# Optimization experiments

Hardware: AMD Instinct MI355X
Metric: run time of the kernel (lower is better)

## Reference

```python
import jax, jax.numpy as jnp
import numpy as np

T, B, S = 128, 64, 256
H, E, V = 1024, 512, 32000
PAD_ID = 0

def setup_inputs() -> dict:
    key = jax.random.key(0)
    ks = jax.random.split(key, 12)
    sc = lambda *sh: 1.0 / np.sqrt(sh[-1])
    return {
        'target_ids': jax.random.randint(ks[0], (T, B), 0, V, dtype=jnp.int32),
        'visual_context': jax.random.normal(ks[1], (B, S, 2 * H), jnp.float32),
        'h0': jax.random.normal(ks[2], (B, H), jnp.float32),
        'c0': jax.random.normal(ks[3], (B, H), jnp.float32),
        'E_tgt': jax.random.normal(ks[4], (V, E), jnp.float32) * 0.02,
        'W_att': jax.random.normal(ks[5], (H, 2 * H), jnp.float32) * sc(2 * H),
        'b_att': jnp.zeros((H,), jnp.float32),
        'W_ih': jax.random.normal(ks[6], (4 * H, E + H), jnp.float32) * sc(E + H),
        'W_hh': jax.random.normal(ks[7], (4 * H, H), jnp.float32) * sc(H),
        'W_u': jax.random.normal(ks[8], (H, 3 * H), jnp.float32) * sc(3 * H),
        'W_vocab': jax.random.normal(ks[9], (V, H), jnp.float32) * sc(H),
        'b_vocab': jnp.zeros((V,), jnp.float32),
    }

def reference(target_ids, visual_context, h0, c0, E_tgt, W_att, b_att,
              W_ih, W_hh, W_u, W_vocab, b_vocab):
    # enc_hidden_proj = att_projection(visual_context): (B, S, H)
    enc_proj = jnp.einsum('bsd,hd->bsh', visual_context, W_att) + b_att
    Y = E_tgt[target_ids[:-1]]  # (T-1, B, E) — teacher-forced inputs

    def step(carry, Y_t):
        h, c, o_prev = carry
        Ybar = jnp.concatenate([o_prev, Y_t], axis=1)  # (B, H+E)
        gates = Ybar @ W_ih.T + h @ W_hh.T             # (B, 4H), no bias
        i, f, g, o = jnp.split(gates, 4, axis=1)       # torch LSTMCell order
        i = jax.nn.sigmoid(i); f = jax.nn.sigmoid(f)
        g = jnp.tanh(g); o = jax.nn.sigmoid(o)
        c = f * c + i * g
        h = o * jnp.tanh(c)
        e_t = jnp.einsum('bsh,bh->bs', enc_proj, h)    # attention scores
        alpha = jax.nn.softmax(e_t, axis=1)
        a_t = jnp.einsum('bs,bsd->bd', alpha, visual_context)  # (B, 2H)
        u_t = jnp.concatenate([a_t, h], axis=1)        # (B, 3H)
        o_t = jnp.tanh(u_t @ W_u.T)                    # dropout = identity (eval)
        return (h, c, o_t), o_t

    o_init = jnp.zeros((h0.shape[0], W_u.shape[0]), h0.dtype)
    _, combined = jax.lax.scan(step, (h0, c0, o_init), Y)  # (T-1, B, H)

    logits = jnp.einsum('tbh,vh->tbv', combined, W_vocab) + b_vocab
    P = jax.nn.log_softmax(logits, axis=-1)            # (T-1, B, V)
    gold = target_ids[1:]                              # (T-1, B)
    gold_lp = jnp.take_along_axis(P, gold[..., None].astype(jnp.int32), axis=-1)[..., 0]
    mask = (gold != PAD_ID).astype(P.dtype)
    scores = (gold_lp * mask).sum(axis=0)              # (B,)
    return scores
```

## Files before the change

kernel.cpp:

```cpp
#include <hip/hip_runtime.h>
#include <hip/hip_bf16.h>

#define TSTEPS 127
#define NBLK 256
#define NVB 250
#define MROWS 8128

typedef unsigned short u16;
typedef unsigned int u32;
typedef unsigned long long u64;
typedef _Float16 f16;
typedef __attribute__((ext_vector_type(8))) short bf16x8;
typedef __attribute__((ext_vector_type(8))) _Float16 f16x8;
typedef __attribute__((ext_vector_type(8))) unsigned short u16x8;
typedef __attribute__((ext_vector_type(4))) float f32x4;

__device__ __forceinline__ u16 f2h(float f){ f16 h=(f16)f; u16 r; __builtin_memcpy(&r,&h,2); return r; }
__device__ __forceinline__ float h2f(u16 u){ f16 h; __builtin_memcpy(&h,&u,2); return (float)h; }
__device__ __forceinline__ float us2f(u16 u){ union{float f;u32 i;}v; v.i=(u32)u<<16; return v.f; }
__device__ __forceinline__ u16 f2us(float f){ __hip_bfloat16 h=__float2bfloat16(f); u16 r; __builtin_memcpy(&r,&h,2); return r; }
__device__ __forceinline__ void split2(float x, u16& hi, u16& lo){
  u16 h = f2us(x); lo = f2us(x - us2f(h)); hi = h;
}

__device__ __forceinline__ u64 ldg64(const u64* p){
  return __hip_atomic_load((u64*)p, __ATOMIC_RELAXED, __HIP_MEMORY_SCOPE_AGENT);
}
__device__ __forceinline__ float ldgf(const float* p){
  return __hip_atomic_load((float*)p, __ATOMIC_RELAXED, __HIP_MEMORY_SCOPE_AGENT);
}
__device__ __forceinline__ void stg64(u64* p, u64 v){
  __hip_atomic_store(p, v, __ATOMIC_RELAXED, __HIP_MEMORY_SCOPE_AGENT);
}
__device__ __forceinline__ void stg32(u32* p, u32 v){
  __hip_atomic_store(p, v, __ATOMIC_RELAXED, __HIP_MEMORY_SCOPE_AGENT);
}
__device__ __forceinline__ void stgf(float* p, float v){
  __hip_atomic_store(p, v, __ATOMIC_RELAXED, __HIP_MEMORY_SCOPE_AGENT);
}
__device__ __forceinline__ f16x8 mk8h(u64 a, u64 b){
  union { u64 q[2]; f16x8 v; } u; u.q[0]=a; u.q[1]=b; return u.v;
}

__device__ __forceinline__ void gbar(u32* flags, u32 token){
  asm volatile("s_waitcnt vmcnt(0) lgkmcnt(0)" ::: "memory");
  __syncthreads();
  if (threadIdx.x == 0)
    __hip_atomic_store(&flags[blockIdx.x*32], token, __ATOMIC_RELAXED, __HIP_MEMORY_SCOPE_AGENT);
  u32* myf = &flags[threadIdx.x*32];
  while (__hip_atomic_load(myf, __ATOMIC_RELAXED, __HIP_MEMORY_SCOPE_AGENT) < token)
    __builtin_amdgcn_s_sleep(1);
  __syncthreads();
}

__global__ void p_wcat(const float* __restrict__ Watt, const float* __restrict__ Wu,
                       float* __restrict__ Wcat){
  int idx = blockIdx.x*256 + threadIdx.x;
  int n = idx >> 11, k = idx & 2047;
  Wcat[idx] = (n < 1024) ? Watt[idx] : Wu[(size_t)(n-1024)*3072 + k];
}

__global__ void p_wy(const float* __restrict__ Wih, u16* __restrict__ WYh, u16* __restrict__ WYl){
  int k = blockIdx.x*256 + threadIdx.x;
  int rp = blockIdx.y;
  int j = (rp & 3)*1024 + (rp >> 2);
  float v = Wih[(size_t)j*1536 + 1024 + k];
  u16 hi, lo; split2(v, hi, lo);
  WYh[(size_t)rp*512 + k] = hi; WYl[(size_t)rp*512 + k] = lo;
}

__global__ void p_wuh(const float* __restrict__ Wu, u16* __restrict__ Wh){
  int k = blockIdx.x*256 + threadIdx.x;
  int j = blockIdx.y;
  Wh[(size_t)j*1024 + k] = f2h(Wu[(size_t)j*3072 + 2048 + k]);
}

__global__ void p_y(const int* __restrict__ ids, const float* __restrict__ Etgt,
                    u16* __restrict__ Yh, u16* __restrict__ Yl){
  int e0 = blockIdx.x*256 + threadIdx.x;
  int row = blockIdx.y;
  int id = ids[row];
  float v = Etgt[(size_t)id*512 + e0];
  u16 hi, lo; split2(v, hi, lo);
  Yh[(size_t)row*512 + e0] = hi; Yl[(size_t)row*512 + e0] = lo;
}

__global__ void p_wv(const float* __restrict__ Wv, u16* __restrict__ Wvb){
  size_t idx = (size_t)blockIdx.x*256 + threadIdx.x;
  Wvb[idx] = f2h(Wv[idx]);
}

__global__ void p_init(const float* __restrict__ h0,
                       u16* __restrict__ hf, u16* __restrict__ of,
                       u32* __restrict__ flags){
  int idx = blockIdx.x*256 + threadIdx.x;
  if (idx < 65536){
    hf[idx] = f2h(h0[idx]);
    of[idx] = 0;
  } else if (idx < 65536 + 8192){
    flags[idx - 65536] = 0;
  }
}

union SharedU {
  struct { u16 a[128*72]; u16 b[128*72]; } st;
  float cc[128*128];
};

__global__ __launch_bounds__(256) void k_gemm32(
    const float* __restrict__ A, const float* __restrict__ Bm,
    const float* __restrict__ bias, u16* __restrict__ ep, u16* __restrict__ vu)
{
  __shared__ SharedU sm;
  const int tid = threadIdx.x;
  const int lane = tid & 63, w = tid >> 6;
  const int wm = w >> 1, wn = w & 1;
  int lw = blockIdx.y * gridDim.x + blockIdx.x;
  int swz = (lw & 7)*256 + (lw >> 3);
  const int n0 = (swz & 15) * 128, m0 = (swz >> 4) * 128;
  f32x4 acc[4][4];
#pragma unroll
  for (int i=0;i<4;i++)
#pragma unroll
    for (int j=0;j<4;j++) acc[i][j] = (f32x4)(0.f);

  for (int k0 = 0; k0 < 2048; k0 += 64) {
    __syncthreads();
#pragma unroll
    for (int i=0;i<8;i++){
      int idx = tid + i*256;
      int r = idx >> 4, c4 = idx & 15;
      float4 va = *(const float4*)(&A[(size_t)(m0+r)*2048 + k0 + c4*4]);
      ushort4 sa; sa.x=f2h(va.x); sa.y=f2h(va.y); sa.z=f2h(va.z); sa.w=f2h(va.w);
      *(ushort4*)(&sm.st.a[r*72 + c4*4]) = sa;
      float4 vb = *(const float4*)(&Bm[(size_t)(n0+r)*2048 + k0 + c4*4]);
      ushort4 sb; sb.x=f2h(vb.x); sb.y=f2h(vb.y); sb.z=f2h(vb.z); sb.w=f2h(vb.w);
      *(ushort4*)(&sm.st.b[r*72 + c4*4]) = sb;
    }
    __syncthreads();
#pragma unroll
    for (int kk = 0; kk < 64; kk += 32) {
      f16x8 af[4], bfr[4];
      int krow = kk + ((lane >> 4) << 3);
#pragma unroll
      for (int m4=0;m4<4;m4++)
        af[m4] = *(const f16x8*)(&sm.st.a[(wm*64 + m4*16 + (lane & 15))*72 + krow]);
#pragma unroll
      for (int n4=0;n4<4;n4++)
        bfr[n4] = *(const f16x8*)(&sm.st.b[(wn*64 + n4*16 + (lane & 15))*72 + krow]);
#pragma unroll
      for (int m4=0;m4<4;m4++)
#pragma unroll
        for (int n4=0;n4<4;n4++)
          acc[m4][n4] = __builtin_amdgcn_mfma_f32_16x16x32_f16(af[m4], bfr[n4], acc[m4][n4], 0,0,0);
    }
  }
  __syncthreads();
#pragma unroll
  for (int m4=0;m4<4;m4++)
#pragma unroll
    for (int n4=0;n4<4;n4++)
#pragma unroll
      for (int i=0;i<4;i++){
        int row = wm*64 + m4*16 + ((lane>>4)<<2) + i;
        int col = wn*64 + n4*16 + (lane&15);
        sm.cc[row*128 + col] = acc[m4][n4][i];
      }
  __syncthreads();
  for (int idx = tid; idx < 128*128; idx += 256) {
    int row = idx >> 7, col = idx & 127;
    int gm = m0 + row, gn = n0 + col;
    float vv = sm.cc[idx];
    if (gn < 1024) { vv += bias[gn]; ep[(size_t)gm*1024 + gn] = f2h(vv); }
    else           { vu[(size_t)gm*1024 + (gn-1024)] = f2h(vv); }
  }
}

__global__ __launch_bounds__(256) void k_gy(
    const u16* __restrict__ Ah, const u16* __restrict__ Al,
    const u16* __restrict__ Bh, const u16* __restrict__ Bl,
    float* __restrict__ gY)
{
  __shared__ u16 sah[128*40], sal[128*40], sbh[128*40], sbl[128*40];
  const int tid = threadIdx.x;
  const int lane = tid & 63, w = tid >> 6;
  const int wm = w >> 1, wn = w & 1;
  const int l15 = lane & 15, q8 = (lane>>4)*8;
  int lw = blockIdx.y * gridDim.x + blockIdx.x;
  int swz = (lw & 7)*256 + (lw >> 3);
  const int n0 = (swz & 31)*128, m0 = (swz >> 5)*128;
  f32x4 acc[4][4];
#pragma unroll
  for (int i=0;i<4;i++)
#pragma unroll
    for (int j=0;j<4;j++) acc[i][j] = (f32x4)(0.f);

  for (int k0 = 0; k0 < 512; k0 += 32){
    __syncthreads();
#pragma unroll
    for (int i=0;i<8;i++){
      int idx = i*256 + tid;
      int mat = idx >> 9, sub = idx & 511;
      int r = sub >> 2, c8 = (sub & 3)*8;
      const u16* src = (mat==0)?Ah:(mat==1)?Al:(mat==2)?Bh:Bl;
      size_t base = (mat<2 ? (size_t)(m0+r)*512 : (size_t)(n0+r)*512) + k0 + c8;
      u16x8 v = *(const u16x8*)(src + base);
      u16* dst = (mat==0)?sah:(mat==1)?sal:(mat==2)?sbh:sbl;
      *(u16x8*)(&dst[r*40 + c8]) = v;
    }
    __syncthreads();
    bf16x8 ah[4], al2[4], bh[4], bl2[4];
#pragma unroll
    for (int m4=0;m4<4;m4++){
      ah[m4]  = *(const bf16x8*)(&sah[(wm*64+m4*16+l15)*40 + q8]);
      al2[m4] = *(const bf16x8*)(&sal[(wm*64+m4*16+l15)*40 + q8]);
    }
#pragma unroll
    for (int n4=0;n4<4;n4++){
      bh[n4]  = *(const bf16x8*)(&sbh[(wn*64+n4*16+l15)*40 + q8]);
      bl2[n4] = *(const bf16x8*)(&sbl[(wn*64+n4*16+l15)*40 + q8]);
    }
#pragma unroll
    for (int m4=0;m4<4;m4++)
#pragma unroll
      for (int n4=0;n4<4;n4++){
        acc[m4][n4] = __builtin_amdgcn_mfma_f32_16x16x32_bf16(ah[m4],  bh[n4],  acc[m4][n4], 0,0,0);
        acc[m4][n4] = __builtin_amdgcn_mfma_f32_16x16x32_bf16(al2[m4], bh[n4],  acc[m4][n4], 0,0,0);
        acc[m4][n4] = __builtin_amdgcn_mfma_f32_16x16x32_bf16(ah[m4],  bl2[n4], acc[m4][n4], 0,0,0);
      }
  }
#pragma unroll
  for (int m4=0;m4<4;m4++)
#pragma unroll
    for (int n4=0;n4<4;n4++)
#pragma unroll
      for (int i=0;i<4;i++){
        int gm = m0 + wm*64 + m4*16 + ((lane>>4)<<2) + i;
        int gn = n0 + wn*64 + n4*16 + l15;
        gY[(size_t)gm*4096 + gn] = acc[m4][n4][i];
      }
}

struct LoopShared {
  u16 wg[32*2048];
  union {
    struct { float psum[2][64][8]; u32 hstage[32][4]; } p1;
    struct { float al[256]; float pared[4][256]; float red[8]; } p3;
  } u;
};

__global__ __launch_bounds__(256, 1) void k_loop(
    const float* __restrict__ Wih, const float* __restrict__ Whh,
    const float* __restrict__ c0g,
    const u16* __restrict__ Wuh16, const float* __restrict__ gY,
    const u16* __restrict__ ep, const u16* __restrict__ vuu,
    u16* __restrict__ hf, u16* __restrict__ of,
    float* __restrict__ ebuf, float* __restrict__ phB,
    u16* __restrict__ comb, u32* __restrict__ flags)
{
  __shared__ LoopShared sh;
  const int tid = threadIdx.x, blk = blockIdx.x;
  const int lane = tid & 63, w = tid >> 6;
  const int l15 = lane & 15, q = lane >> 4;
  const int jb = blk >> 1, bhalf = blk & 1;
  const int bsub = w & 1, khalf = w >> 1;
  const int b = bhalf*32 + bsub*16 + l15;

  for (int i = tid; i < 32*512; i += 256){
    int r = i >> 9, c4 = i & 511;
    int jp = jb*32 + r;
    int j  = (jp & 3)*1024 + (jp >> 2);
    float4 v = (c4 < 256) ? *(const float4*)(&Wih[(size_t)j*1536 + c4*4])
                          : *(const float4*)(&Whh[(size_t)j*1024 + (c4-256)*4]);
    ushort4 hh; hh.x=f2h(v.x); hh.y=f2h(v.y); hh.z=f2h(v.z); hh.w=f2h(v.w);
    int byteoff = (r*4096 + c4*8) ^ ((r & 7) << 4);
    *(ushort4*)((char*)sh.wg + byteoff) = hh;
  }
  float cReg0 = 0.f, cReg1 = 0.f;
  if (w < 2){
    cReg0 = c0g[(size_t)b*1024 + jb*8 + q];
    cReg1 = c0g[(size_t)b*1024 + jb*8 + 4 + q];
  }
  __syncthreads();
  const char* wgc = (const char*)sh.wg;

  for (int t = 0; t < TSTEPS; ++t){
    const int p = t & 1;
    const u16* hP = hf + p*65536;
    u16* hN = hf + (p^1)*65536;

    {
      float4 gyv0, gyv1;
      if (w < 2){
        const float* gb = gY + ((size_t)(t*64 + b))*4096 + jb*32 + q*4;
        gyv0 = *(const float4*)(gb);
        gyv1 = *(const float4*)(gb + 16);
      }
      const u64* xsrc = (khalf ? (const u64*)hP : (const u64*)of) + b*256;
      f32x4 acc0 = (f32x4)(0.f), acc1 = (f32x4)(0.f);
#pragma unroll 4
      for (int kt = 0; kt < 32; ++kt){
        int base = khalf*2048 + kt*64 + q*16;
        int w0 = (l15*4096 + base) ^ ((l15 & 7) << 4);
        f16x8 wf0 = *(const f16x8*)(wgc + w0);
        f16x8 wf1 = *(const f16x8*)(wgc + w0 + 65536);
        const u64* px = xsrc + kt*8 + q*2;
        f16x8 xf = mk8h(ldg64(px), ldg64(px+1));
        acc0 = __builtin_amdgcn_mfma_f32_16x16x32_f16(wf0, xf, acc0, 0,0,0);
        acc1 = __builtin_amdgcn_mfma_f32_16x16x32_f16(wf1, xf, acc1, 0,0,0);
      }
      if (w >= 2){
        float* ps_ = &sh.u.p1.psum[w-2][lane][0];
#pragma unroll
        for (int i=0;i<4;i++){ ps_[i] = acc0[i]; ps_[4+i] = acc1[i]; }
      }
      __syncthreads();
      if (w < 2){
        const float* ps_ = &sh.u.p1.psum[w][lane][0];
        u16 h0b, h1b;
        {
          float gi = acc0[0]+ps_[0]+gyv0.x, gf = acc0[1]+ps_[1]+gyv0.y;
          float gg = acc0[2]+ps_[2]+gyv0.z, go = acc0[3]+ps_[3]+gyv0.w;
          gi = 1.f/(1.f+expf(-gi)); gf = 1.f/(1.f+expf(-gf));
          gg = tanhf(gg);           go = 1.f/(1.f+expf(-go));
          float cn = gf*cReg0 + gi*gg; cReg0 = cn;
          h0b = f2h(go*tanhf(cn));
        }
        {
          float gi = acc1[0]+ps_[4]+gyv1.x, gf = acc1[1]+ps_[5]+gyv1.y;
          float gg = acc1[2]+ps_[6]+gyv1.z, go = acc1[3]+ps_[7]+gyv1.w;
          gi = 1.f/(1.f+expf(-gi)); gf = 1.f/(1.f+expf(-gf));
          gg = tanhf(gg);           go = 1.f/(1.f+expf(-go));
          float cn = gf*cReg1 + gi*gg; cReg1 = cn;
          h1b = f2h(go*tanhf(cn));
        }
        int bl = bsub*16 + l15;
        u16* hs = (u16*)sh.u.p1.hstage;
        hs[bl*8 + q] = h0b;
        hs[bl*8 + 4 + q] = h1b;
      }
      __syncthreads();
      if (tid < 128){
        int bl = tid >> 2, sub = tid & 3;
        u32 v = sh.u.p1.hstage[bl][sub];
        stg32((u32*)hN + (size_t)(bhalf*32 + bl)*512 + jb*4 + sub, v);
      }
    }
    gbar(flags, (u32)(t*3 + 1));

    if (blk < 16){
      const int jrow = blk*64 + w*16 + l15;
      const u16* wp = Wuh16 + (size_t)jrow*1024;
      f32x4 pacc[4];
#pragma unroll
      for (int i=0;i<4;i++) pacc[i] = (f32x4)(0.f);
#pragma unroll 2
      for (int kt = 0; kt < 32; ++kt){
        f16x8 bfr = *(const f16x8*)(wp + kt*32 + q*8);
#pragma unroll
        for (int m=0;m<4;m++){
          const u64* px = (const u64*)hN + (size_t)(m*16+l15)*256 + kt*8 + q*2;
          f16x8 xf = mk8h(ldg64(px), ldg64(px+1));
          pacc[m] = __builtin_amdgcn_mfma_f32_16x16x32_f16(xf, bfr, pacc[m], 0,0,0);
        }
      }
#pragma unroll
      for (int m=0;m<4;m++)
#pragma unroll
        for (int i=0;i<4;i++){
          int bb = m*16 + q*4 + i;
          stgf(phB + (size_t)bb*1024 + jrow, pacc[m][i]);
        }
    } else {
      for (int u2 = blk - 16; u2 < 256; u2 += 240){
        const int ab = u2 >> 2, sl = u2 & 3;
        float hr[64];
        {
          const u64* hp = (const u64*)hN + (size_t)ab*256 + l15*16;
#pragma unroll
          for (int i=0;i<16;i++){
            union{u64 q_; u16 s[4];} uu; uu.q_ = ldg64(hp + i);
#pragma unroll
            for (int e=0;e<4;e++) hr[i*4+e] = h2f(uu.s[e]);
          }
        }
        const int rbase = sl*64 + w*16;
#pragma unroll
        for (int rg = 0; rg < 4; rg++){
          int s = rbase + rg*4 + q;
          const u16x8* row = (const u16x8*)(ep + ((size_t)(ab*256 + s))*1024 + l15*64);
          float a = 0.f;
#pragma unroll
          for (int j=0;j<8;j++){
            u16x8 v = row[j];
#pragma unroll
            for (int e=0;e<8;e++) a += h2f(v[e]) * hr[j*8+e];
          }
          a += __shfl_xor(a, 1); a += __shfl_xor(a, 2);
          a += __shfl_xor(a, 4); a += __shfl_xor(a, 8);
          if (l15 == 0) stgf(ebuf + ab*256 + s, a);
        }
      }
    }
    gbar(flags, (u32)(t*3 + 2));

    {
      const int ab = blk >> 2, jq = blk & 3;
      float x = ldgf(ebuf + ab*256 + tid);
      float m_ = x;
#pragma unroll
      for (int off=32; off; off>>=1) m_ = fmaxf(m_, __shfl_xor(m_, off));
      if (lane == 0) sh.u.p3.red[w] = m_;
      __syncthreads();
      m_ = fmaxf(fmaxf(sh.u.p3.red[0],sh.u.p3.red[1]), fmaxf(sh.u.p3.red[2],sh.u.p3.red[3]));
      float pv = expf(x - m_);
      float sv = pv;
#pragma unroll
      for (int off=32; off; off>>=1) sv += __shfl_xor(sv, off);
      if (lane == 0) sh.u.p3.red[4+w] = sv;
      __syncthreads();
      float tot = sh.u.p3.red[4]+sh.u.p3.red[5]+sh.u.p3.red[6]+sh.u.p3.red[7];
      sh.u.p3.al[tid] = pv / tot;
      __syncthreads();
      float a0=0.f, a1=0.f, a2=0.f, a3=0.f;
      const u16* vb = vuu + ((size_t)(ab*256) + w*64)*1024 + jq*256 + lane*4;
      for (int s2=0; s2<64; s2++){
        float aa = sh.u.p3.al[w*64 + s2];
        ushort4 v = *(const ushort4*)(vb + (size_t)s2*1024);
        a0 += aa*h2f(v.x); a1 += aa*h2f(v.y); a2 += aa*h2f(v.z); a3 += aa*h2f(v.w);
      }
      float4 o4; o4.x=a0; o4.y=a1; o4.z=a2; o4.w=a3;
      *(float4*)(&sh.u.p3.pared[w][lane*4]) = o4;
      __syncthreads();
      if (tid < 64){
        const int col = tid*4;
        union{u64 q_; u16 s[4];} uo;
        ushort4 cw;
#pragma unroll
        for (int i=0;i<4;i++){
          float pa = sh.u.p3.pared[0][col+i] + sh.u.p3.pared[1][col+i]
                   + sh.u.p3.pared[2][col+i] + sh.u.p3.pared[3][col+i];
          pa += ldgf(phB + (size_t)ab*1024 + jq*256 + col + i);
          u16 ob = f2h(tanhf(pa));
          uo.s[i] = ob; (&cw.x)[i] = ob;
        }
        stg64((u64*)of + (size_t)ab*256 + jq*64 + tid, uo.q_);
        *(ushort4*)(comb + (size_t)(t*64 + ab)*1024 + jq*256 + col) = cw;
      }
    }
    gbar(flags, (u32)(t*3 + 3));
  }
}

__global__ __launch_bounds__(256) void k_gemm16(
    const u16* __restrict__ A, const u16* __restrict__ Bm,
    const float* __restrict__ bias,
    float* __restrict__ pm, float* __restrict__ ps,
    float* __restrict__ gl, const int* __restrict__ ids)
{
  __shared__ SharedU sm;
  const int tid = threadIdx.x;
  const int lane = tid & 63, w = tid >> 6;
  const int wm = w >> 1, wn = w & 1;
  int lw = blockIdx.y * 250 + blockIdx.x;
  int swz = (lw & 7)*2000 + (lw >> 3);
  const int n0 = (swz % 250) * 128, m0 = (swz / 250) * 128;
  f32x4 acc[4][4];
#pragma unroll
  for (int i=0;i<4;i++)
#pragma unroll
    for (int j=0;j<4;j++) acc[i][j] = (f32x4)(0.f);

  for (int k0 = 0; k0 < 1024; k0 += 64) {
    __syncthreads();
#pragma unroll
    for (int i=0;i<8;i++){
      int idx = i*256 + tid;
      int half = idx >> 10, id2 = idx & 1023;
      int r = id2 >> 3, c8 = (id2 & 7)*8;
      if (half == 0){
        int gm = m0 + r;
        u16x8 v = {0,0,0,0,0,0,0,0};
        if (gm < MROWS) v = *(const u16x8*)(A + (size_t)gm*1024 + k0 + c8);
        *(u16x8*)(&sm.st.a[r*72 + c8]) = v;
      } else {
        u16x8 v = *(const u16x8*)(Bm + (size_t)(n0 + r)*1024 + k0 + c8);
        *(u16x8*)(&sm.st.b[r*72 + c8]) = v;
      }
    }
    __syncthreads();
#pragma unroll
    for (int kk = 0; kk < 64; kk += 32) {
      f16x8 af[4], bfr[4];
      int krow = kk + ((lane >> 4) << 3);
#pragma unroll
      for (int m4=0;m4<4;m4++)
        af[m4] = *(const f16x8*)(&sm.st.a[(wm*64 + m4*16 + (lane & 15))*72 + krow]);
#pragma unroll
      for (int n4=0;n4<4;n4++)
        bfr[n4] = *(const f16x8*)(&sm.st.b[(wn*64 + n4*16 + (lane & 15))*72 + krow]);
#pragma unroll
      for (int m4=0;m4<4;m4++)
#pragma unroll
        for (int n4=0;n4<4;n4++)
          acc[m4][n4] = __builtin_amdgcn_mfma_f32_16x16x32_f16(af[m4], bfr[n4], acc[m4][n4], 0,0,0);
    }
  }
  __syncthreads();
#pragma unroll
  for (int m4=0;m4<4;m4++)
#pragma unroll
    for (int n4=0;n4<4;n4++)
#pragma unroll
      for (int i=0;i<4;i++){
        int row = wm*64 + m4*16 + ((lane>>4)<<2) + i;
        int col = wn*64 + n4*16 + (lane&15);
        sm.cc[row*128 + col] = acc[m4][n4][i];
      }
  __syncthreads();

  if (tid < 128) {
    int row = tid, gm = m0 + row;
    if (gm < MROWS) {
      float mx = -1e30f;
      for (int j=0;j<128;j++){
        int col = (row + j) & 127;
        float x = sm.cc[row*128+col] + bias[n0+col];
        mx = fmaxf(mx, x);
      }
      float sum = 0.f;
      for (int j=0;j<128;j++){
        int col = (row + j) & 127;
        float x = sm.cc[row*128+col] + bias[n0+col];
        sum += expf(x - mx);
      }
      pm[(size_t)gm*NVB + n0/128] = mx;
      ps[(size_t)gm*NVB + n0/128] = sum;
      int g = ids[gm + 64];
      unsigned d = (unsigned)(g - n0);
      if (d < 128u) gl[gm] = sm.cc[row*128 + (int)d] + bias[g];
    }
  }
}

__global__ void k_reduce(const float* __restrict__ pm, const float* __restrict__ ps,
                         const float* __restrict__ gl, const int* __restrict__ ids,
                         float* __restrict__ out)
{
  int b = blockIdx.x, tid = threadIdx.x;
  int lane = tid & 63, w = tid >> 6;
  __shared__ float wacc[4];
  float accum = 0.f;
  for (int t = w; t < TSTEPS; t += 4) {
    int r = t*64 + b;
    const float* pmr = pm + (size_t)r*NVB;
    const float* psr = ps + (size_t)r*NVB;
    float mx = -1e30f;
    for (int p2 = lane; p2 < NVB; p2 += 64) mx = fmaxf(mx, pmr[p2]);
#pragma unroll
    for (int off=32; off; off>>=1) mx = fmaxf(mx, __shfl_xor(mx, off));
    float sm = 0.f;
    for (int p2 = lane; p2 < NVB; p2 += 64) sm += psr[p2] * expf(pmr[p2] - mx);
#pragma unroll
    for (int off=32; off; off>>=1) sm += __shfl_xor(sm, off);
    if (lane == 0) {
      int g = ids[r + 64];
      if (g != 0) accum += gl[r] - (mx + logf(sm));
    }
  }
  if (lane == 0) wacc[w] = accum;
  __syncthreads();
  if (tid == 0) out[b] = wacc[0]+wacc[1]+wacc[2]+wacc[3];
}

extern "C" void kernel_launch(void* const* d_in, const int* in_sizes, int n_in,
                              void* d_out, int out_size, void* d_ws, size_t ws_size,
                              hipStream_t stream)
{
  const int*   ids  = (const int*)d_in[0];
  const float* vc   = (const float*)d_in[1];
  const float* h0   = (const float*)d_in[2];
  const float* c0   = (const float*)d_in[3];
  const float* Etgt = (const float*)d_in[4];
  const float* Watt = (const float*)d_in[5];
  const float* batt = (const float*)d_in[6];
  const float* Wih  = (const float*)d_in[7];
  const float* Whh  = (const float*)d_in[8];
  const float* Wu   = (const float*)d_in[9];
  const float* Wv   = (const float*)d_in[10];
  const float* bv   = (const float*)d_in[11];
  float* out = (float*)d_out;

  char* p = (char*)d_ws;
  auto alloc = [&](size_t bytes)->char* {
    char* r = p; p += (bytes + 255) & ~(size_t)255; return r;
  };
  u32* flags = (u32*)alloc(32768);
  u16* Yh    = (u16*)alloc((size_t)8192*512*2);
  u16* Yl    = (u16*)alloc((size_t)8192*512*2);
  u16* WYh   = (u16*)alloc((size_t)4096*512*2);
  u16* WYl   = (u16*)alloc((size_t)4096*512*2);
  u16* Wuh16 = (u16*)alloc((size_t)1024*1024*2);
  float* Wcat= (float*)alloc((size_t)2048*2048*4);
  u16* ep    = (u16*)alloc((size_t)64*256*1024*2);
  u16* vuu   = (u16*)alloc((size_t)64*256*1024*2);
  u16* Wvb   = (u16*)alloc((size_t)32000*1024*2);
  u16* comb  = (u16*)alloc((size_t)8192*1024*2);
  float* gY  = (float*)alloc((size_t)8192*4096*4);
  u16* hfbuf = (u16*)alloc((size_t)2*65536*2);
  u16* ofbuf = (u16*)alloc(65536*2);
  float* ebuf= (float*)alloc((size_t)64*256*4);
  float* phB = (float*)alloc((size_t)64*1024*4);
  float* pm  = (float*)alloc((size_t)MROWS*NVB*4);
  float* ps  = (float*)alloc((size_t)MROWS*NVB*4);
  float* gl  = (float*)alloc((size_t)MROWS*4);

  p_init<<<288, 256, 0, stream>>>(h0, hfbuf, ofbuf, flags);
  p_wcat<<<(2048*2048)/256, 256, 0, stream>>>(Watt, Wu, Wcat);
  p_wy<<<dim3(2, 4096), 256, 0, stream>>>(Wih, WYh, WYl);
  p_wuh<<<dim3(4, 1024), 256, 0, stream>>>(Wu, Wuh16);
  p_y<<<dim3(2, 8192), 256, 0, stream>>>(ids, Etgt, Yh, Yl);
  p_wv<<<(32000*1024)/256, 256, 0, stream>>>(Wv, Wvb);

  k_gemm32<<<dim3(16, 128), 256, 0, stream>>>(vc, Wcat, batt, ep, vuu);
  k_gy<<<dim3(32, 64), 256, 0, stream>>>(Yh, Yl, WYh, WYl, gY);

  k_loop<<<NBLK, 256, 0, stream>>>(Wih, Whh, c0, Wuh16, gY, ep, vuu,
                                   hfbuf, ofbuf, ebuf, phB, comb, flags);

  k_gemm16<<<dim3(NVB, 64), 256, 0, stream>>>(comb, Wvb, bv, pm, ps, gl, ids);
  k_reduce<<<64, 256, 0, stream>>>(pm, ps, gl, ids, out);
}
```

Baseline: 13.37 ms.

## Double persistent loop block size to 512 threads and split work across eight waves

After: 14.67 ms. 9.7% more time.

```diff
diff --git a/kernel.cpp b/kernel.cpp
--- a/kernel.cpp
+++ b/kernel.cpp
@@ -47,7 +47,7 @@
   __syncthreads();
   if (threadIdx.x == 0)
     __hip_atomic_store(&flags[blockIdx.x*32], token, __ATOMIC_RELAXED, __HIP_MEMORY_SCOPE_AGENT);
-  u32* myf = &flags[threadIdx.x*32];
+  u32* myf = &flags[(threadIdx.x & 255)*32];
   while (__hip_atomic_load(myf, __ATOMIC_RELAXED, __HIP_MEMORY_SCOPE_AGENT) < token)
     __builtin_amdgcn_s_sleep(1);
   __syncthreads();
@@ -244,12 +244,12 @@
 struct LoopShared {
   u16 wg[32*2048];
   union {
-    struct { float psum[2][64][8]; u32 hstage[32][4]; } p1;
-    struct { float al[256]; float pared[4][256]; float red[8]; } p3;
+    struct { float psum[6][64][8]; u32 hstage[32][4]; } p1;
+    struct { float al[256]; float pared[8][256]; float red[8]; float red2[8]; } p3;
   } u;
 };
 
-__global__ __launch_bounds__(256, 1) void k_loop(
+__global__ __launch_bounds__(512, 2) void k_loop(
     const float* __restrict__ Wih, const float* __restrict__ Whh,
     const float* __restrict__ c0g,
     const u16* __restrict__ Wuh16, const float* __restrict__ gY,
@@ -263,10 +263,10 @@
   const int lane = tid & 63, w = tid >> 6;
   const int l15 = lane & 15, q = lane >> 4;
   const int jb = blk >> 1, bhalf = blk & 1;
-  const int bsub = w & 1, khalf = w >> 1;
+  const int bsub = w & 1, kq = w >> 1;
   const int b = bhalf*32 + bsub*16 + l15;
 
-  for (int i = tid; i < 32*512; i += 256){
+  for (int i = tid; i < 32*512; i += 512){
     int r = i >> 9, c4 = i & 511;
     int jp = jb*32 + r;
     int j  = (jp & 3)*1024 + (jp >> 2);
@@ -296,12 +296,11 @@
         gyv0 = *(const float4*)(gb);
         gyv1 = *(const float4*)(gb + 16);
       }
-      const u64* xsrc = (khalf ? (const u64*)hP : (const u64*)of) + b*256;
+      const u64* xsrc = (kq < 2 ? (const u64*)of : (const u64*)hP) + b*256 + (kq & 1)*128;
       f32x4 acc0 = (f32x4)(0.f), acc1 = (f32x4)(0.f);
 #pragma unroll 4
-      for (int kt = 0; kt < 32; ++kt){
-        int base = khalf*2048 + kt*64 + q*16;
-        int w0 = (l15*4096 + base) ^ ((l15 & 7) << 4);
+      for (int kt = 0; kt < 16; ++kt){
+        int w0 = (l15*4096 + kq*1024 + kt*64 + q*16) ^ ((l15 & 7) << 4);
         f16x8 wf0 = *(const f16x8*)(wgc + w0);
         f16x8 wf1 = *(const f16x8*)(wgc + w0 + 65536);
         const u64* px = xsrc + kt*8 + q*2;
@@ -316,19 +315,25 @@
       }
       __syncthreads();
       if (w < 2){
-        const float* ps_ = &sh.u.p1.psum[w][lane][0];
+        const float* p0 = &sh.u.p1.psum[bsub][lane][0];
+        const float* p1_ = &sh.u.p1.psum[2+bsub][lane][0];
+        const float* p2_ = &sh.u.p1.psum[4+bsub][lane][0];
         u16 h0b, h1b;
         {
-          float gi = acc0[0]+ps_[0]+gyv0.x, gf = acc0[1]+ps_[1]+gyv0.y;
-          float gg = acc0[2]+ps_[2]+gyv0.z, go = acc0[3]+ps_[3]+gyv0.w;
+          float gi = acc0[0]+p0[0]+p1_[0]+p2_[0]+gyv0.x;
+          float gf = acc0[1]+p0[1]+p1_[1]+p2_[1]+gyv0.y;
+          float gg = acc0[2]+p0[2]+p1_[2]+p2_[2]+gyv0.z;
+          float go = acc0[3]+p0[3]+p1_[3]+p2_[3]+gyv0.w;
           gi = 1.f/(1.f+expf(-gi)); gf = 1.f/(1.f+expf(-gf));
           gg = tanhf(gg);           go = 1.f/(1.f+expf(-go));
           float cn = gf*cReg0 + gi*gg; cReg0 = cn;
           h0b = f2h(go*tanhf(cn));
         }
         {
-          float gi = acc1[0]+ps_[4]+gyv1.x, gf = acc1[1]+ps_[5]+gyv1.y;
-          float gg = acc1[2]+ps_[6]+gyv1.z, go = acc1[3]+ps_[7]+gyv1.w;
+          float gi = acc1[0]+p0[4]+p1_[4]+p2_[4]+gyv1.x;
+          float gf = acc1[1]+p0[5]+p1_[5]+p2_[5]+gyv1.y;
+          float gg = acc1[2]+p0[6]+p1_[6]+p2_[6]+gyv1.z;
+          float go = acc1[3]+p0[7]+p1_[7]+p2_[7]+gyv1.w;
           gi = 1.f/(1.f+expf(-gi)); gf = 1.f/(1.f+expf(-gf));
           gg = tanhf(gg);           go = 1.f/(1.f+expf(-go));
           float cn = gf*cReg1 + gi*gg; cReg1 = cn;
@@ -348,8 +353,8 @@
     }
     gbar(flags, (u32)(t*3 + 1));
 
-    if (blk < 16){
-      const int jrow = blk*64 + w*16 + l15;
+    if (blk < 8){
+      const int jrow = blk*128 + w*16 + l15;
       const u16* wp = Wuh16 + (size_t)jrow*1024;
       f32x4 pacc[4];
 #pragma unroll
@@ -372,33 +377,35 @@
           stgf(phB + (size_t)bb*1024 + jrow, pacc[m][i]);
         }
     } else {
-      for (int u2 = blk - 16; u2 < 256; u2 += 240){
+      for (int u2 = blk - 8; u2 < 256; u2 += 248){
         const int ab = u2 >> 2, sl = u2 & 3;
-        float hr[64];
+        float hr[16];
         {
-          const u64* hp = (const u64*)hN + (size_t)ab*256 + l15*16;
-#pragma unroll
-          for (int i=0;i<16;i++){
-            union{u64 q_; u16 s[4];} uu; uu.q_ = ldg64(hp + i);
-#pragma unroll
-            for (int e=0;e<4;e++) hr[i*4+e] = h2f(uu.s[e]);
+          const u64* hp = (const u64*)hN + (size_t)ab*256;
+          union{u64 q_; u16 s[4];} ua, ub2;
+#pragma unroll
+          for (int hv=0; hv<2; hv++){
+            ua.q_  = ldg64(hp + lane*2 + hv);
+            ub2.q_ = ldg64(hp + 128 + lane*2 + hv);
+#pragma unroll
+            for (int e=0;e<4;e++){ hr[hv*4+e] = h2f(ua.s[e]); hr[8+hv*4+e] = h2f(ub2.s[e]); }
           }
         }
-        const int rbase = sl*64 + w*16;
-#pragma unroll
-        for (int rg = 0; rg < 4; rg++){
-          int s = rbase + rg*4 + q;
-          const u16x8* row = (const u16x8*)(ep + ((size_t)(ab*256 + s))*1024 + l15*64);
+#pragma unroll
+        for (int rr = 0; rr < 8; rr++){
+          int s = sl*64 + w*8 + rr;
+          const u16x8* row = (const u16x8*)(ep + ((size_t)(ab*256 + s))*1024);
+          u16x8 v1 = row[lane];
+          u16x8 v2 = row[lane + 64];
           float a = 0.f;
 #pragma unroll
-          for (int j=0;j<8;j++){
-            u16x8 v = row[j];
-#pragma unroll
-            for (int e=0;e<8;e++) a += h2f(v[e]) * hr[j*8+e];
-          }
-          a += __shfl_xor(a, 1); a += __shfl_xor(a, 2);
-          a += __shfl_xor(a, 4); a += __shfl_xor(a, 8);
-          if (l15 == 0) stgf(ebuf + ab*256 + s, a);
+          for (int e=0;e<8;e++) a += h2f(v1[e]) * hr[e];
+#pragma unroll
+          for (int e=0;e<8;e++) a += h2f(v2[e]) * hr[8+e];
+          a += __shfl_xor(a, 1);  a += __shfl_xor(a, 2);
+          a += __shfl_xor(a, 4);  a += __shfl_xor(a, 8);
+          a += __shfl_xor(a, 16); a += __shfl_xor(a, 32);
+          if (lane == 0) stgf(ebuf + ab*256 + s, a);
         }
       }
     }
@@ -406,26 +413,31 @@
 
     {
       const int ab = blk >> 2, jq = blk & 3;
-      float x = ldgf(ebuf + ab*256 + tid);
+      float x = ldgf(ebuf + ab*256 + (tid & 255));
       float m_ = x;
 #pragma unroll
       for (int off=32; off; off>>=1) m_ = fmaxf(m_, __shfl_xor(m_, off));
       if (lane == 0) sh.u.p3.red[w] = m_;
       __syncthreads();
-      m_ = fmaxf(fmaxf(sh.u.p3.red[0],sh.u.p3.red[1]), fmaxf(sh.u.p3.red[2],sh.u.p3.red[3]));
+      m_ = sh.u.p3.red[0];
+#pragma unroll
+      for (int i=1;i<8;i++) m_ = fmaxf(m_, sh.u.p3.red[i]);
       float pv = expf(x - m_);
       float sv = pv;
 #pragma unroll
       for (int off=32; off; off>>=1) sv += __shfl_xor(sv, off);
-      if (lane == 0) sh.u.p3.red[4+w] = sv;
+      if (lane == 0) sh.u.p3.red2[w] = sv;
       __syncthreads();
-      float tot = sh.u.p3.red[4]+sh.u.p3.red[5]+sh.u.p3.red[6]+sh.u.p3.red[7];
-      sh.u.p3.al[tid] = pv / tot;
+      float tot = 0.f;
+#pragma unroll
+      for (int i=0;i<8;i++) tot += sh.u.p3.red2[i];
+      tot *= 0.5f;
+      sh.u.p3.al[tid & 255] = pv / tot;
       __syncthreads();
       float a0=0.f, a1=0.f, a2=0.f, a3=0.f;
-      const u16* vb = vuu + ((size_t)(ab*256) + w*64)*1024 + jq*256 + lane*4;
-      for (int s2=0; s2<64; s2++){
-        float aa = sh.u.p3.al[w*64 + s2];
+      const u16* vb = vuu + ((size_t)(ab*256) + w*32)*1024 + jq*256 + lane*4;
+      for (int s2=0; s2<32; s2++){
+        float aa = sh.u.p3.al[w*32 + s2];
         ushort4 v = *(const ushort4*)(vb + (size_t)s2*1024);
         a0 += aa*h2f(v.x); a1 += aa*h2f(v.y); a2 += aa*h2f(v.z); a3 += aa*h2f(v.w);
       }
@@ -438,8 +450,9 @@
         ushort4 cw;
 #pragma unroll
         for (int i=0;i<4;i++){
-          float pa = sh.u.p3.pared[0][col+i] + sh.u.p3.pared[1][col+i]
-                   + sh.u.p3.pared[2][col+i] + sh.u.p3.pared[3][col+i];
+          float pa = 0.f;
+#pragma unroll
+          for (int ww=0; ww<8; ww++) pa += sh.u.p3.pared[ww][col+i];
           pa += ldgf(phB + (size_t)ab*1024 + jq*256 + col + i);
           u16 ob = f2h(tanhf(pa));
           uo.s[i] = ob; (&cw.x)[i] = ob;
@@ -625,7 +638,7 @@
   k_gemm32<<<dim3(16, 128), 256, 0, stream>>>(vc, Wcat, batt, ep, vuu);
   k_gy<<<dim3(32, 64), 256, 0, stream>>>(Yh, Yl, WYh, WYl, gY);
 
-  k_loop<<<NBLK, 256, 0, stream>>>(Wih, Whh, c0, Wuh16, gY, ep, vuu,
+  k_loop<<<NBLK, 512, 0, stream>>>(Wih, Whh, c0, Wuh16, gY, ep, vuu,
                                    hfbuf, ofbuf, ebuf, phB, comb, flags);
 
   k_gemm16<<<dim3(NVB, 64), 256, 0, stream>>>(comb, Wvb, bv, pm, ps, gl, ids);
```

## Store gY in fp16, fuse vocab weight conversion into GEMM, poll barrier with one wave

Applied to the files above, without the earlier changes.

New measurement: 13.56 ms. About the same (+1.4%).

```diff
diff --git a/kernel.cpp b/kernel.cpp
--- a/kernel.cpp
+++ b/kernel.cpp
@@ -47,9 +47,17 @@
   __syncthreads();
   if (threadIdx.x == 0)
     __hip_atomic_store(&flags[blockIdx.x*32], token, __ATOMIC_RELAXED, __HIP_MEMORY_SCOPE_AGENT);
-  u32* myf = &flags[threadIdx.x*32];
-  while (__hip_atomic_load(myf, __ATOMIC_RELAXED, __HIP_MEMORY_SCOPE_AGENT) < token)
-    __builtin_amdgcn_s_sleep(1);
+  if (threadIdx.x < 64){
+    const int l = threadIdx.x;
+    for (;;){
+      bool ok = true;
+#pragma unroll
+      for (int i=0;i<4;i++)
+        ok &= (__hip_atomic_load(&flags[(l*4+i)*32], __ATOMIC_RELAXED, __HIP_MEMORY_SCOPE_AGENT) >= token);
+      if (__all(ok)) break;
+      __builtin_amdgcn_s_sleep(8);
+    }
+  }
   __syncthreads();
 }
 
@@ -83,11 +91,6 @@
   float v = Etgt[(size_t)id*512 + e0];
   u16 hi, lo; split2(v, hi, lo);
   Yh[(size_t)row*512 + e0] = hi; Yl[(size_t)row*512 + e0] = lo;
-}
-
-__global__ void p_wv(const float* __restrict__ Wv, u16* __restrict__ Wvb){
-  size_t idx = (size_t)blockIdx.x*256 + threadIdx.x;
-  Wvb[idx] = f2h(Wv[idx]);
 }
 
 __global__ void p_init(const float* __restrict__ h0,
@@ -179,7 +182,7 @@
 __global__ __launch_bounds__(256) void k_gy(
     const u16* __restrict__ Ah, const u16* __restrict__ Al,
     const u16* __restrict__ Bh, const u16* __restrict__ Bl,
-    float* __restrict__ gY)
+    u16* __restrict__ gY)
 {
   __shared__ u16 sah[128*40], sal[128*40], sbh[128*40], sbl[128*40];
   const int tid = threadIdx.x;
@@ -237,7 +240,7 @@
       for (int i=0;i<4;i++){
         int gm = m0 + wm*64 + m4*16 + ((lane>>4)<<2) + i;
         int gn = n0 + wn*64 + n4*16 + l15;
-        gY[(size_t)gm*4096 + gn] = acc[m4][n4][i];
+        gY[(size_t)gm*4096 + gn] = f2h(acc[m4][n4][i]);
       }
 }
 
@@ -252,7 +255,7 @@
 __global__ __launch_bounds__(256, 1) void k_loop(
     const float* __restrict__ Wih, const float* __restrict__ Whh,
     const float* __restrict__ c0g,
-    const u16* __restrict__ Wuh16, const float* __restrict__ gY,
+    const u16* __restrict__ Wuh16, const u16* __restrict__ gY,
     const u16* __restrict__ ep, const u16* __restrict__ vuu,
     u16* __restrict__ hf, u16* __restrict__ of,
     float* __restrict__ ebuf, float* __restrict__ phB,
@@ -290,11 +293,13 @@
     u16* hN = hf + (p^1)*65536;
 
     {
-      float4 gyv0, gyv1;
+      float gy0[4], gy1[4];
       if (w < 2){
-        const float* gb = gY + ((size_t)(t*64 + b))*4096 + jb*32 + q*4;
-        gyv0 = *(const float4*)(gb);
-        gyv1 = *(const float4*)(gb + 16);
+        const u16* gb = gY + ((size_t)(t*64 + b))*4096 + jb*32 + q*4;
+        ushort4 g0 = *(const ushort4*)(gb);
+        ushort4 g1 = *(const ushort4*)(gb + 16);
+        gy0[0]=h2f(g0.x); gy0[1]=h2f(g0.y); gy0[2]=h2f(g0.z); gy0[3]=h2f(g0.w);
+        gy1[0]=h2f(g1.x); gy1[1]=h2f(g1.y); gy1[2]=h2f(g1.z); gy1[3]=h2f(g1.w);
       }
       const u64* xsrc = (khalf ? (const u64*)hP : (const u64*)of) + b*256;
       f32x4 acc0 = (f32x4)(0.f), acc1 = (f32x4)(0.f);
@@ -319,16 +324,16 @@
         const float* ps_ = &sh.u.p1.psum[w][lane][0];
         u16 h0b, h1b;
         {
-          float gi = acc0[0]+ps_[0]+gyv0.x, gf = acc0[1]+ps_[1]+gyv0.y;
-          float gg = acc0[2]+ps_[2]+gyv0.z, go = acc0[3]+ps_[3]+gyv0.w;
+          float gi = acc0[0]+ps_[0]+gy0[0], gf = acc0[1]+ps_[1]+gy0[1];
+          float gg = acc0[2]+ps_[2]+gy0[2], go = acc0[3]+ps_[3]+gy0[3];
           gi = 1.f/(1.f+expf(-gi)); gf = 1.f/(1.f+expf(-gf));
           gg = tanhf(gg);           go = 1.f/(1.f+expf(-go));
           float cn = gf*cReg0 + gi*gg; cReg0 = cn;
           h0b = f2h(go*tanhf(cn));
         }
         {
-          float gi = acc1[0]+ps_[4]+gyv1.x, gf = acc1[1]+ps_[5]+gyv1.y;
-          float gg = acc1[2]+ps_[6]+gyv1.z, go = acc1[3]+ps_[7]+gyv1.w;
+          float gi = acc1[0]+ps_[4]+gy1[0], gf = acc1[1]+ps_[5]+gy1[1];
+          float gg = acc1[2]+ps_[6]+gy1[2], go = acc1[3]+ps_[7]+gy1[3];
           gi = 1.f/(1.f+expf(-gi)); gf = 1.f/(1.f+expf(-gf));
           gg = tanhf(gg);           go = 1.f/(1.f+expf(-go));
           float cn = gf*cReg1 + gi*gg; cReg1 = cn;
@@ -453,7 +458,7 @@
 }
 
 __global__ __launch_bounds__(256) void k_gemm16(
-    const u16* __restrict__ A, const u16* __restrict__ Bm,
+    const u16* __restrict__ A, const float* __restrict__ Bm,
     const float* __restrict__ bias,
     float* __restrict__ pm, float* __restrict__ ps,
     float* __restrict__ gl, const int* __restrict__ ids)
@@ -484,8 +489,13 @@
         if (gm < MROWS) v = *(const u16x8*)(A + (size_t)gm*1024 + k0 + c8);
         *(u16x8*)(&sm.st.a[r*72 + c8]) = v;
       } else {
-        u16x8 v = *(const u16x8*)(Bm + (size_t)(n0 + r)*1024 + k0 + c8);
-        *(u16x8*)(&sm.st.b[r*72 + c8]) = v;
+        const float* src = Bm + (size_t)(n0 + r)*1024 + k0 + c8;
+        float4 a4 = *(const float4*)src;
+        float4 b4 = *(const float4*)(src + 4);
+        ushort4 ha; ha.x=f2h(a4.x); ha.y=f2h(a4.y); ha.z=f2h(a4.z); ha.w=f2h(a4.w);
+        ushort4 hb; hb.x=f2h(b4.x); hb.y=f2h(b4.y); hb.z=f2h(b4.z); hb.w=f2h(b4.w);
+        *(ushort4*)(&sm.st.b[r*72 + c8]) = ha;
+        *(ushort4*)(&sm.st.b[r*72 + c8 + 4]) = hb;
       }
     }
     __syncthreads();
@@ -604,9 +614,8 @@
   float* Wcat= (float*)alloc((size_t)2048*2048*4);
   u16* ep    = (u16*)alloc((size_t)64*256*1024*2);
   u16* vuu   = (u16*)alloc((size_t)64*256*1024*2);
-  u16* Wvb   = (u16*)alloc((size_t)32000*1024*2);
   u16* comb  = (u16*)alloc((size_t)8192*1024*2);
-  float* gY  = (float*)alloc((size_t)8192*4096*4);
+  u16* gY    = (u16*)alloc((size_t)8192*4096*2);
   u16* hfbuf = (u16*)alloc((size_t)2*65536*2);
   u16* ofbuf = (u16*)alloc(65536*2);
   float* ebuf= (float*)alloc((size_t)64*256*4);
@@ -620,7 +629,6 @@
   p_wy<<<dim3(2, 4096), 256, 0, stream>>>(Wih, WYh, WYl);
   p_wuh<<<dim3(4, 1024), 256, 0, stream>>>(Wu, Wuh16);
   p_y<<<dim3(2, 8192), 256, 0, stream>>>(ids, Etgt, Yh, Yl);
-  p_wv<<<(32000*1024)/256, 256, 0, stream>>>(Wv, Wvb);
 
   k_gemm32<<<dim3(16, 128), 256, 0, stream>>>(vc, Wcat, batt, ep, vuu);
   k_gy<<<dim3(32, 64), 256, 0, stream>>>(Yh, Yl, WYh, WYl, gY);
@@ -628,6 +636,6 @@
   k_loop<<<NBLK, 256, 0, stream>>>(Wih, Whh, c0, Wuh16, gY, ep, vuu,
                                    hfbuf, ofbuf, ebuf, phB, comb, flags);
 
-  k_gemm16<<<dim3(NVB, 64), 256, 0, stream>>>(comb, Wvb, bv, pm, ps, gl, ids);
+  k_gemm16<<<dim3(NVB, 64), 256, 0, stream>>>(comb, Wv, bv, pm, ps, gl, ids);
   k_reduce<<<64, 256, 0, stream>>>(pm, ps, gl, ids, out);
 }
```
